# Performance work log

Measured on AMD Instinct MI355X. Metric: run time of the kernel, lower is better.

## Reference

```python
import jax, jax.numpy as jnp
import numpy as np

EPS = float(np.finfo(np.float64).eps)  # matches np.finfo(float).eps in torch combine()
TOP_K = 2


def setup_inputs() -> dict:
    key = jax.random.key(0)
    k0, k1, k2, k3 = jax.random.split(key, 4)
    N, D, F, E = 8192, 512, 2048, 8
    s = 0.02  # init scale keeps exp() in combine numerically tame
    return {
        "x": jax.random.normal(k0, (N, D), jnp.float32),
        "Wg": jax.random.normal(k1, (D, E), jnp.float32) * s,
        "W1": jax.random.normal(k2, (E, D, F), jnp.float32) * s,
        "b1": jnp.zeros((E, F), jnp.float32),
        "W2": jax.random.normal(k3, (E, F, D), jnp.float32) * s,
        "b2": jnp.zeros((E, D), jnp.float32),
    }


def reference(x, Wg, W1, b1, W2, b2):
    """Sparse-MoE token routing: gate -> dispatch -> per-expert MLP -> combine.

    Faithful to the torch dispatch()/combine() helpers: experts produce
    log-domain outputs; combine() does exp, gate-weighted scatter-add, eps
    floor, then log. Here expressed as dense masked expert compute (zero
    gates annihilate non-routed contributions), which is mathematically
    identical to the gather/index_add formulation and fully vectorized.
    """
    N, D = x.shape
    E = Wg.shape[1]
    # --- gating: noisy-free top-k softmax gates, scattered to [N, E] ---
    logits = x @ Wg                                    # [N, E]
    top_vals, top_idx = jax.lax.top_k(logits, TOP_K)   # [N, K]
    top_gates = jax.nn.softmax(top_vals, axis=-1)      # [N, K]
    gates = jnp.zeros((N, E), x.dtype).at[jnp.arange(N)[:, None], top_idx].set(top_gates)
    # --- expert MLPs (ReLU, per activation='relu' default) ---
    h = jax.nn.relu(jnp.einsum('nd,edf->nef', x, W1) + b1[None])  # [N, E, F]
    o = jnp.einsum('nef,efd->ned', h, W2) + b2[None]              # [N, E, D]
    # --- combine: gate-weighted sum of exp(expert_out), eps floor, log ---
    combined = jnp.einsum('ne,ned->nd', gates, jnp.exp(o))        # [N, D]
    combined = jnp.where(combined == 0, EPS, combined)
    return jnp.log(combined)
```

## Files before the change

kernel.cpp:

```cpp
#include <hip/hip_runtime.h>
#include <stdint.h>
#include <math.h>

#define NTOK 8192
#define DIM  512
#define FDIM 2048
#define NEXP 8
#define RMAX 17408
#define NMT  136
#define KSPLIT 2

typedef __attribute__((ext_vector_type(8))) __bf16 bf16x8;
typedef __attribute__((ext_vector_type(4))) float  f32x4;

#define GTPB 16
#define GB_BLOCKS (NTOK / GTPB)
#define PREP_W1 (GB_BLOCKS)
#define PREP_W2 (GB_BLOCKS + 8192)

#define OFF_W1T    ((size_t)0)
#define SZ_W1T     ((size_t)NEXP * DIM * FDIM * 2)
#define OFF_W2T    (OFF_W1T + SZ_W1T)
#define SZ_W2T     SZ_W1T
#define OFF_H      (OFF_W2T + SZ_W2T)
#define SZ_H       ((size_t)RMAX * FDIM * 2)
#define OFF_META   (OFF_H + SZ_H)
#define SZ_META    ((size_t)1024)
#define OFF_XG     (OFF_META + SZ_META)
#define SZ_XG      ((size_t)RMAX * DIM * 2)
#define OFF_O1     OFF_XG
#define OFF_O0     (OFF_XG + SZ_XG)
#define SZ_O0      ((size_t)RMAX * DIM * 4)
#define OFF_TOKE   (OFF_O0 + SZ_O0)
#define OFF_TOKLS  (OFF_TOKE + (size_t)NTOK * 8)
#define OFF_TOKG   (OFF_TOKLS + (size_t)NTOK * 8)
#define OFF_HISTP  (OFF_TOKG + (size_t)NTOK * 8)
#define OFF_BASEP  (OFF_HISTP + (size_t)GB_BLOCKS * NEXP * 4)
#define OFF_ROWS   (OFF_BASEP + (size_t)GB_BLOCKS * NEXP * 4)

__device__ __forceinline__ unsigned short f2bf(float f) {
  union { float f; unsigned int u; } v; v.f = f;
  unsigned int u = v.u;
  return (unsigned short)((u + 0x7fffu + ((u >> 16) & 1u)) >> 16);
}
__device__ __forceinline__ float bf2f(unsigned short u) {
  union { unsigned int u; float f; } v; v.u = ((unsigned int)u) << 16;
  return v.f;
}

__device__ __forceinline__ void gld16(const unsigned short* g, unsigned short* l) {
  __builtin_amdgcn_global_load_lds(
      (const __attribute__((address_space(1))) void*)g,
      (__attribute__((address_space(3))) void*)l, 16, 0, 0);
}

__device__ __forceinline__ void transpose_tile(const float* __restrict__ src,
                                               unsigned short* __restrict__ dst,
                                               int R, int C, int bx, int by, int bz) {
  __shared__ float t[32][33];
  const int r0 = by * 32, c0 = bx * 32;
  const float* s = src + (size_t)bz * R * C;
  unsigned short* d = dst + (size_t)bz * R * C;
  const int tr = threadIdx.x >> 5, tc = threadIdx.x & 31;
  #pragma unroll
  for (int i = 0; i < 4; i++)
    t[tr + i * 8][tc] = s[(size_t)(r0 + tr + i * 8) * C + (c0 + tc)];
  __syncthreads();
  #pragma unroll
  for (int i = 0; i < 4; i++)
    d[(size_t)(c0 + tr + i * 8) * R + (r0 + tc)] = f2bf(t[tc][tr + i * 8]);
}

__device__ __forceinline__ void gate_body(int gb, const float* __restrict__ x,
                            const float* __restrict__ Wg,
                            int* __restrict__ hist_part, int2* __restrict__ tok_e,
                            int2* __restrict__ tok_ls, float2* __restrict__ tok_g) {
  __shared__ int hist[NEXP];
  __shared__ int le[GTPB][2];
  __shared__ int ls[GTPB][2];
  __shared__ float lg[GTPB][2];
  const int wid = threadIdx.x >> 6;
  const int lane = threadIdx.x & 63;
  if (threadIdx.x < NEXP) hist[threadIdx.x] = 0;
  __syncthreads();
  for (int t = 0; t < 4; t++) {
    const int lt = wid * 4 + t;
    const int n = gb * GTPB + lt;
    double acc[NEXP];
    #pragma unroll
    for (int e = 0; e < NEXP; e++) acc[e] = 0.0;
    #pragma unroll
    for (int i = 0; i < 8; i++) {
      int dd = lane + i * 64;
      double xv = (double)x[(size_t)n * DIM + dd];
      const float* wr = Wg + (size_t)dd * NEXP;
      #pragma unroll
      for (int e = 0; e < NEXP; e++) acc[e] += xv * (double)wr[e];
    }
    #pragma unroll
    for (int s = 32; s > 0; s >>= 1)
      #pragma unroll
      for (int e = 0; e < NEXP; e++) acc[e] += __shfl_xor(acc[e], s, 64);
    if (lane == 0) {
      int i0 = 0;
      #pragma unroll
      for (int e = 1; e < NEXP; e++) if (acc[e] > acc[i0]) i0 = e;
      int i1 = (i0 == 0) ? 1 : 0;
      #pragma unroll
      for (int e = 0; e < NEXP; e++) { if (e == i0 || e == i1) continue; if (acc[e] > acc[i1]) i1 = e; }
      double e1 = exp(acc[i1] - acc[i0]), ssum = 1.0 + e1;
      le[lt][0] = i0; le[lt][1] = i1;
      ls[lt][0] = atomicAdd(&hist[i0], 1);
      ls[lt][1] = atomicAdd(&hist[i1], 1);
      lg[lt][0] = (float)(1.0 / ssum); lg[lt][1] = (float)(e1 / ssum);
    }
  }
  __syncthreads();
  if (threadIdx.x < NEXP) hist_part[gb * NEXP + threadIdx.x] = hist[threadIdx.x];
  if (threadIdx.x < GTPB) {
    const int lt = threadIdx.x;
    const int n = gb * GTPB + lt;
    tok_e[n]  = make_int2(le[lt][0], le[lt][1]);
    tok_ls[n] = make_int2(ls[lt][0], ls[lt][1]);
    tok_g[n]  = make_float2(lg[lt][0], lg[lt][1]);
  }
}

__global__ __launch_bounds__(256) void prep_kernel(const float* __restrict__ W1,
    unsigned short* __restrict__ W1t, const float* __restrict__ W2,
    unsigned short* __restrict__ W2t, const float* __restrict__ x,
    const float* __restrict__ Wg, int* __restrict__ hist_part, int2* __restrict__ tok_e,
    int2* __restrict__ tok_ls, float2* __restrict__ tok_g) {
  const int b = blockIdx.x;
  if (b < GB_BLOCKS) {
    gate_body(b, x, Wg, hist_part, tok_e, tok_ls, tok_g);
  } else if (b < PREP_W2) {
    const int q = b - PREP_W1;
    transpose_tile(W1, W1t, DIM, FDIM, q & 63, (q >> 6) & 15, q >> 10);
  } else {
    const int q = b - PREP_W2;
    transpose_tile(W2, W2t, FDIM, DIM, q & 15, (q >> 4) & 63, q >> 10);
  }
}

__global__ __launch_bounds__(256) void scan_kernel(const int* __restrict__ hist_part,
    int* __restrict__ offsets, int* __restrict__ base_part, int* __restrict__ mtile_e) {
  __shared__ int hp[GB_BLOCKS * NEXP];
  __shared__ int segsum[8][NEXP];
  __shared__ int segbase[8][NEXP];
  __shared__ int tot[NEXP];
  __shared__ int soff[NEXP + 1];
  for (int i = threadIdx.x; i < GB_BLOCKS * NEXP; i += 256) hp[i] = hist_part[i];
  __syncthreads();
  if (threadIdx.x < 64) {
    const int e = threadIdx.x & 7, s = threadIdx.x >> 3;
    int run = 0;
    for (int b = s * 64; b < s * 64 + 64; b++) {
      int v = hp[b * NEXP + e]; hp[b * NEXP + e] = run; run += v;
    }
    segsum[s][e] = run;
  }
  __syncthreads();
  if (threadIdx.x < NEXP) {
    const int e = threadIdx.x;
    int run = 0;
    for (int s = 0; s < 8; s++) { segbase[s][e] = run; run += segsum[s][e]; }
    tot[e] = run;
  }
  __syncthreads();
  if (threadIdx.x == 0) {
    int off = 0;
    for (int e = 0; e < NEXP; e++) { soff[e] = off; offsets[e] = off; off += (tot[e] + 127) & ~127; }
    soff[NEXP] = off; offsets[NEXP] = off;
    for (int t = 0; t < NMT; t++) {
      int r = t * 128, e = NEXP - 1;
      for (int q = 0; q < NEXP; q++)
        if (r >= soff[q] && r < soff[q + 1]) { e = q; break; }
      mtile_e[t] = e;
    }
  }
  __syncthreads();
  for (int i = threadIdx.x; i < GB_BLOCKS * NEXP; i += 256) {
    const int b = i >> 3, e = i & 7;
    base_part[i] = soff[e] + segbase[b >> 6][e] + hp[i];
  }
}

__global__ void gather_kernel(const float* __restrict__ x, const int2* __restrict__ tok_e,
                              const int2* __restrict__ tok_ls, const int* __restrict__ base_part,
                              ushort4* __restrict__ xg, int2* __restrict__ rows) {
  const int n = blockIdx.x;
  int2 te = tok_e[n]; int2 tl = tok_ls[n];
  const int gb = n / GTPB;
  const int r0 = base_part[gb * NEXP + te.x] + tl.x;
  const int r1 = base_part[gb * NEXP + te.y] + tl.y;
  if (threadIdx.x == 0) rows[n] = make_int2(r0, r1);
  const float4* xr = (const float4*)(x + (size_t)n * DIM);
  float4 v = xr[threadIdx.x];
  ushort4 o;
  o.x = f2bf(v.x); o.y = f2bf(v.y); o.z = f2bf(v.z); o.w = f2bf(v.w);
  xg[(size_t)r0 * (DIM / 4) + threadIdx.x] = o;
  xg[(size_t)r1 * (DIM / 4) + threadIdx.x] = o;
}

template <int K, int LDA, int LDB>
__device__ __forceinline__ void gemm_core(const unsigned short* __restrict__ A,
                                          const unsigned short* __restrict__ B,
                                          int m0, int n0, f32x4 acc[4][4]) {
  __shared__ __align__(16) unsigned short As[128 * 64];
  __shared__ __align__(16) unsigned short Bs[128 * 64];
  const int tid = threadIdx.x;
  const int wid = tid >> 6, lane = tid & 63;
  const int wm = (wid >> 1) * 64, wn = (wid & 1) * 64;
  const int quad = lane >> 4, l16 = lane & 15;
  const int srow = tid >> 3;
  const int scol = ((tid & 7) ^ (srow & 7)) << 3;
  unsigned short* As_w = As + 512 * wid;
  unsigned short* Bs_w = Bs + 512 * wid;
  const int r7 = (l16 & 7) << 3;
  const unsigned short* Ar = A + (size_t)(m0 + srow) * LDA + scol;
  const unsigned short* Br = B + (size_t)(n0 + srow) * LDB + scol;
  #pragma unroll 1
  for (int kt = 0; kt < K; kt += 64) {
    __syncthreads();
    #pragma unroll
    for (int p = 0; p < 4; p++) {
      gld16(Ar + (size_t)(32 * p) * LDA + kt, As_w + p * 2048);
      gld16(Br + (size_t)(32 * p) * LDB + kt, Bs_w + p * 2048);
    }
    __syncthreads();
    #pragma unroll
    for (int kk = 0; kk < 2; kk++) {
      const int swz = ((kk * 4 + quad) << 3) ^ r7;
      bf16x8 af[4], bfr[4];
      #pragma unroll
      for (int i = 0; i < 4; i++) {
        af[i]  = *(const bf16x8*)(As + (wm + i * 16 + l16) * 64 + swz);
        bfr[i] = *(const bf16x8*)(Bs + (wn + i * 16 + l16) * 64 + swz);
      }
      #pragma unroll
      for (int mi = 0; mi < 4; mi++)
        #pragma unroll
        for (int ni = 0; ni < 4; ni++)
          acc[mi][ni] = __builtin_amdgcn_mfma_f32_16x16x32_bf16(af[mi], bfr[ni], acc[mi][ni], 0, 0, 0);
    }
  }
}

__global__ __launch_bounds__(256, 4) void gemm1_kernel(const unsigned short* __restrict__ xg,
    const unsigned short* __restrict__ W1t, const int* __restrict__ mtile_e,
    const float* __restrict__ b1, unsigned short* __restrict__ h) {
  const int bm = blockIdx.x, bn = blockIdx.y;
  const int e = mtile_e[bm];
  f32x4 acc[4][4];
  #pragma unroll
  for (int i = 0; i < 4; i++)
    #pragma unroll
    for (int j = 0; j < 4; j++) acc[i][j] = (f32x4){0.f, 0.f, 0.f, 0.f};
  gemm_core<DIM, DIM, DIM>(xg, W1t + (size_t)e * FDIM * DIM, bm * 128, bn * 128, acc);
  const int tid = threadIdx.x, wid = tid >> 6, lane = tid & 63;
  const int wm = (wid >> 1) * 64, wn = (wid & 1) * 64, quad = lane >> 4, l16 = lane & 15;
  #pragma unroll
  for (int mi = 0; mi < 4; mi++) {
    #pragma unroll
    for (int ni = 0; ni < 4; ni++) {
      const int col = bn * 128 + wn + ni * 16 + l16;
      const float bb = b1[e * FDIM + col];
      #pragma unroll
      for (int r = 0; r < 4; r++) {
        const int row = bm * 128 + wm + mi * 16 + quad * 4 + r;
        float v = acc[mi][ni][r] + bb;
        h[(size_t)row * FDIM + col] = f2bf(v > 0.f ? v : 0.f);
      }
    }
  }
}

__global__ __launch_bounds__(256, 4) void gemm2_kernel(const unsigned short* __restrict__ h,
    const unsigned short* __restrict__ W2t, const int* __restrict__ mtile_e,
    float* __restrict__ o0, unsigned short* __restrict__ o1) {
  const int bm = blockIdx.x, bn = blockIdx.y, ks = blockIdx.z;
  const int e = mtile_e[bm];
  const int k0 = ks * (FDIM / KSPLIT);
  f32x4 acc[4][4];
  #pragma unroll
  for (int i = 0; i < 4; i++)
    #pragma unroll
    for (int j = 0; j < 4; j++) acc[i][j] = (f32x4){0.f, 0.f, 0.f, 0.f};
  gemm_core<FDIM / KSPLIT, FDIM, FDIM>(h + k0, W2t + (size_t)e * DIM * FDIM + k0,
                                       bm * 128, bn * 128, acc);
  const int tid = threadIdx.x, wid = tid >> 6, lane = tid & 63;
  const int wm = (wid >> 1) * 64, wn = (wid & 1) * 64, quad = lane >> 4, l16 = lane & 15;
  if (ks == 0) {
    #pragma unroll
    for (int mi = 0; mi < 4; mi++)
      #pragma unroll
      for (int r = 0; r < 4; r++) {
        const int row = bm * 128 + wm + mi * 16 + quad * 4 + r;
        #pragma unroll
        for (int ni = 0; ni < 4; ni++) {
          const int col = bn * 128 + wn + ni * 16 + l16;
          o0[(size_t)row * DIM + col] = acc[mi][ni][r];
        }
      }
  } else {
    #pragma unroll
    for (int mi = 0; mi < 4; mi++)
      #pragma unroll
      for (int r = 0; r < 4; r++) {
        const int row = bm * 128 + wm + mi * 16 + quad * 4 + r;
        #pragma unroll
        for (int ni = 0; ni < 4; ni++) {
          const int col = bn * 128 + wn + ni * 16 + l16;
          o1[(size_t)row * DIM + col] = f2bf(acc[mi][ni][r]);
        }
      }
  }
}

__global__ void combine_kernel(const float* __restrict__ o0, const unsigned short* __restrict__ o1,
                               const int2* __restrict__ tok_e, const int2* __restrict__ rows,
                               const float2* __restrict__ tok_g, const float* __restrict__ b2,
                               float* __restrict__ out) {
  const int n = blockIdx.x;
  const int c = threadIdx.x * 4;
  int2 te = tok_e[n]; int2 rr = rows[n]; float2 tg = tok_g[n];
  const int r0 = rr.x, r1 = rr.y;
  float4 a0 = *(const float4*)(o0 + (size_t)r0 * DIM + c);
  float4 a1 = *(const float4*)(o0 + (size_t)r1 * DIM + c);
  ushort4 p0 = *(const ushort4*)(o1 + (size_t)r0 * DIM + c);
  ushort4 p1 = *(const ushort4*)(o1 + (size_t)r1 * DIM + c);
  float4 c0 = *(const float4*)(b2 + te.x * DIM + c);
  float4 c1 = *(const float4*)(b2 + te.y * DIM + c);
  float4 res;
  #pragma unroll
  for (int j = 0; j < 4; j++) {
    float v0 = ((const float*)&a0)[j] + bf2f(((const unsigned short*)&p0)[j]) + ((const float*)&c0)[j];
    float v1 = ((const float*)&a1)[j] + bf2f(((const unsigned short*)&p1)[j]) + ((const float*)&c1)[j];
    float v = tg.x * expf(v0) + tg.y * expf(v1);
    v = (v == 0.0f) ? 2.220446049250313e-16f : v;
    ((float*)&res)[j] = logf(v);
  }
  *(float4*)(out + (size_t)n * DIM + c) = res;
}

extern "C" void kernel_launch(void* const* d_in, const int* in_sizes, int n_in,
                              void* d_out, int out_size, void* d_ws, size_t ws_size,
                              hipStream_t stream) {
  const float* x  = (const float*)d_in[0];
  const float* Wg = (const float*)d_in[1];
  const float* W1 = (const float*)d_in[2];
  const float* b1 = (const float*)d_in[3];
  const float* W2 = (const float*)d_in[4];
  const float* b2 = (const float*)d_in[5];
  float* out = (float*)d_out;
  char* ws = (char*)d_ws;

  unsigned short* W1t = (unsigned short*)(ws + OFF_W1T);
  unsigned short* W2t = (unsigned short*)(ws + OFF_W2T);
  unsigned short* h   = (unsigned short*)(ws + OFF_H);
  int* meta    = (int*)(ws + OFF_META);
  int* offsets = meta;
  int* mtile_e = meta + 16;
  unsigned short* xg = (unsigned short*)(ws + OFF_XG);
  unsigned short* o1 = (unsigned short*)(ws + OFF_O1);
  float* o0      = (float*)(ws + OFF_O0);
  int2* tok_e    = (int2*)(ws + OFF_TOKE);
  int2* tok_ls   = (int2*)(ws + OFF_TOKLS);
  float2* tok_g  = (float2*)(ws + OFF_TOKG);
  int* hist_part = (int*)(ws + OFF_HISTP);
  int* base_part = (int*)(ws + OFF_BASEP);
  int2* rows     = (int2*)(ws + OFF_ROWS);

  prep_kernel<<<GB_BLOCKS + 2 * 8192, 256, 0, stream>>>(W1, W1t, W2, W2t, x, Wg,
                                                        hist_part, tok_e, tok_ls, tok_g);
  scan_kernel<<<1, 256, 0, stream>>>(hist_part, offsets, base_part, mtile_e);
  gather_kernel<<<NTOK, 128, 0, stream>>>(x, tok_e, tok_ls, base_part, (ushort4*)xg, rows);
  gemm1_kernel<<<dim3(NMT, FDIM / 128), 256, 0, stream>>>(xg, W1t, mtile_e, b1, h);
  gemm2_kernel<<<dim3(NMT, DIM / 128, KSPLIT), 256, 0, stream>>>(h, W2t, mtile_e, o0, o1);
  combine_kernel<<<NTOK, 128, 0, stream>>>(o0, o1, tok_e, rows, tok_g, b2, out);
}
```

Baseline: 294.3 us.

## Fuse gather into GEMM1 via row indices, skip empty tiles, widen transposes

The separate gather kernel is gone. x is converted to bf16 once inside the gating blocks, and GEMM1 loads A rows indirectly through a token-row map (trow) using global_load_lds, so the duplicated xg buffer is never written. M-tiles that hold only padding are marked -1 and skipped in both GEMMs. The weight transposes use 64x64 tiles with fewer blocks, combine packs two tokens per 256-thread block and uses fast __expf/__logf, and part of the fp32 split-K output reuses the W1t region to save workspace. Risks include precision loss from the fast math intrinsics and the aliasing of o0lo with W1t, which is only safe because GEMM1 has finished before GEMM2 writes.

```diff
diff --git a/kernel.cpp b/kernel.cpp
--- a/kernel.cpp
+++ b/kernel.cpp
@@ -9,6 +9,7 @@
 #define RMAX 17408
 #define NMT  136
 #define KSPLIT 2
+#define O0LO_ROWS 8192
 
 typedef __attribute__((ext_vector_type(8))) __bf16 bf16x8;
 typedef __attribute__((ext_vector_type(4))) float  f32x4;
@@ -16,7 +17,8 @@
 #define GTPB 16
 #define GB_BLOCKS (NTOK / GTPB)
 #define PREP_W1 (GB_BLOCKS)
-#define PREP_W2 (GB_BLOCKS + 8192)
+#define PREP_W2 (GB_BLOCKS + 2048)
+#define PREP_TOTAL (GB_BLOCKS + 4096)
 
 #define OFF_W1T    ((size_t)0)
 #define SZ_W1T     ((size_t)NEXP * DIM * FDIM * 2)
@@ -26,12 +28,14 @@
 #define SZ_H       ((size_t)RMAX * FDIM * 2)
 #define OFF_META   (OFF_H + SZ_H)
 #define SZ_META    ((size_t)1024)
-#define OFF_XG     (OFF_META + SZ_META)
-#define SZ_XG      ((size_t)RMAX * DIM * 2)
-#define OFF_O1     OFF_XG
-#define OFF_O0     (OFF_XG + SZ_XG)
-#define SZ_O0      ((size_t)RMAX * DIM * 4)
-#define OFF_TOKE   (OFF_O0 + SZ_O0)
+#define OFF_XB     (OFF_META + SZ_META)
+#define SZ_XB      ((size_t)NTOK * DIM * 2)
+#define OFF_O1     (OFF_XB + SZ_XB)
+#define SZ_O1      ((size_t)RMAX * DIM * 2)
+#define OFF_O0HI   (OFF_O1 + SZ_O1)
+#define SZ_O0HI    ((size_t)(RMAX - O0LO_ROWS) * DIM * 4)
+#define OFF_TROW   (OFF_O0HI + SZ_O0HI)
+#define OFF_TOKE   (OFF_TROW + (size_t)RMAX * 4)
 #define OFF_TOKLS  (OFF_TOKE + (size_t)NTOK * 8)
 #define OFF_TOKG   (OFF_TOKLS + (size_t)NTOK * 8)
 #define OFF_HISTP  (OFF_TOKG + (size_t)NTOK * 8)
@@ -54,27 +58,28 @@
       (__attribute__((address_space(3))) void*)l, 16, 0, 0);
 }
 
-__device__ __forceinline__ void transpose_tile(const float* __restrict__ src,
-                                               unsigned short* __restrict__ dst,
-                                               int R, int C, int bx, int by, int bz) {
-  __shared__ float t[32][33];
-  const int r0 = by * 32, c0 = bx * 32;
+__device__ __forceinline__ void transpose_tile64(const float* __restrict__ src,
+                                                 unsigned short* __restrict__ dst,
+                                                 int R, int C, int bx, int by, int bz) {
+  __shared__ float t[64][65];
+  const int r0 = by * 64, c0 = bx * 64;
   const float* s = src + (size_t)bz * R * C;
   unsigned short* d = dst + (size_t)bz * R * C;
-  const int tr = threadIdx.x >> 5, tc = threadIdx.x & 31;
-  #pragma unroll
-  for (int i = 0; i < 4; i++)
-    t[tr + i * 8][tc] = s[(size_t)(r0 + tr + i * 8) * C + (c0 + tc)];
-  __syncthreads();
-  #pragma unroll
-  for (int i = 0; i < 4; i++)
-    d[(size_t)(c0 + tr + i * 8) * R + (r0 + tc)] = f2bf(t[tc][tr + i * 8]);
+  const int tr = threadIdx.x >> 6, tc = threadIdx.x & 63;
+  #pragma unroll
+  for (int i = 0; i < 16; i++)
+    t[tr + i * 4][tc] = s[(size_t)(r0 + tr + i * 4) * C + (c0 + tc)];
+  __syncthreads();
+  #pragma unroll
+  for (int i = 0; i < 16; i++)
+    d[(size_t)(c0 + tr + i * 4) * R + (r0 + tc)] = f2bf(t[tc][tr + i * 4]);
 }
 
 __device__ __forceinline__ void gate_body(int gb, const float* __restrict__ x,
                             const float* __restrict__ Wg,
                             int* __restrict__ hist_part, int2* __restrict__ tok_e,
-                            int2* __restrict__ tok_ls, float2* __restrict__ tok_g) {
+                            int2* __restrict__ tok_ls, float2* __restrict__ tok_g,
+                            ushort4* __restrict__ xb) {
   __shared__ int hist[NEXP];
   __shared__ int le[GTPB][2];
   __shared__ int ls[GTPB][2];
@@ -115,6 +120,14 @@
       lg[lt][0] = (float)(1.0 / ssum); lg[lt][1] = (float)(e1 / ssum);
     }
   }
+  for (int v = threadIdx.x; v < GTPB * (DIM / 4); v += 256) {
+    const int lt = v / (DIM / 4), c = v % (DIM / 4);
+    const int n = gb * GTPB + lt;
+    float4 f = *(const float4*)(x + (size_t)n * DIM + c * 4);
+    ushort4 o;
+    o.x = f2bf(f.x); o.y = f2bf(f.y); o.z = f2bf(f.z); o.w = f2bf(f.w);
+    xb[(size_t)n * (DIM / 4) + c] = o;
+  }
   __syncthreads();
   if (threadIdx.x < NEXP) hist_part[gb * NEXP + threadIdx.x] = hist[threadIdx.x];
   if (threadIdx.x < GTPB) {
@@ -130,26 +143,28 @@
     unsigned short* __restrict__ W1t, const float* __restrict__ W2,
     unsigned short* __restrict__ W2t, const float* __restrict__ x,
     const float* __restrict__ Wg, int* __restrict__ hist_part, int2* __restrict__ tok_e,
-    int2* __restrict__ tok_ls, float2* __restrict__ tok_g) {
+    int2* __restrict__ tok_ls, float2* __restrict__ tok_g, ushort4* __restrict__ xb) {
   const int b = blockIdx.x;
   if (b < GB_BLOCKS) {
-    gate_body(b, x, Wg, hist_part, tok_e, tok_ls, tok_g);
+    gate_body(b, x, Wg, hist_part, tok_e, tok_ls, tok_g, xb);
   } else if (b < PREP_W2) {
     const int q = b - PREP_W1;
-    transpose_tile(W1, W1t, DIM, FDIM, q & 63, (q >> 6) & 15, q >> 10);
+    transpose_tile64(W1, W1t, DIM, FDIM, q & 31, (q >> 5) & 7, q >> 8);
   } else {
     const int q = b - PREP_W2;
-    transpose_tile(W2, W2t, FDIM, DIM, q & 15, (q >> 4) & 63, q >> 10);
+    transpose_tile64(W2, W2t, FDIM, DIM, q & 7, (q >> 3) & 31, q >> 8);
   }
 }
 
 __global__ __launch_bounds__(256) void scan_kernel(const int* __restrict__ hist_part,
-    int* __restrict__ offsets, int* __restrict__ base_part, int* __restrict__ mtile_e) {
+    int* __restrict__ offsets, int* __restrict__ base_part, int* __restrict__ mtile_e,
+    int* __restrict__ trow) {
   __shared__ int hp[GB_BLOCKS * NEXP];
   __shared__ int segsum[8][NEXP];
   __shared__ int segbase[8][NEXP];
   __shared__ int tot[NEXP];
   __shared__ int soff[NEXP + 1];
+  for (int i = threadIdx.x; i < RMAX; i += 256) trow[i] = 0;
   for (int i = threadIdx.x; i < GB_BLOCKS * NEXP; i += 256) hp[i] = hist_part[i];
   __syncthreads();
   if (threadIdx.x < 64) {
@@ -176,7 +191,7 @@
       int r = t * 128, e = NEXP - 1;
       for (int q = 0; q < NEXP; q++)
         if (r >= soff[q] && r < soff[q + 1]) { e = q; break; }
-      mtile_e[t] = e;
+      mtile_e[t] = (r < soff[e] + tot[e]) ? e : -1;
     }
   }
   __syncthreads();
@@ -186,21 +201,17 @@
   }
 }
 
-__global__ void gather_kernel(const float* __restrict__ x, const int2* __restrict__ tok_e,
-                              const int2* __restrict__ tok_ls, const int* __restrict__ base_part,
-                              ushort4* __restrict__ xg, int2* __restrict__ rows) {
-  const int n = blockIdx.x;
+__global__ __launch_bounds__(256) void resolve_kernel(const int2* __restrict__ tok_e,
+    const int2* __restrict__ tok_ls, const int* __restrict__ base_part,
+    int2* __restrict__ rows, int* __restrict__ trow) {
+  const int n = blockIdx.x * 256 + threadIdx.x;
   int2 te = tok_e[n]; int2 tl = tok_ls[n];
   const int gb = n / GTPB;
   const int r0 = base_part[gb * NEXP + te.x] + tl.x;
   const int r1 = base_part[gb * NEXP + te.y] + tl.y;
-  if (threadIdx.x == 0) rows[n] = make_int2(r0, r1);
-  const float4* xr = (const float4*)(x + (size_t)n * DIM);
-  float4 v = xr[threadIdx.x];
-  ushort4 o;
-  o.x = f2bf(v.x); o.y = f2bf(v.y); o.z = f2bf(v.z); o.w = f2bf(v.w);
-  xg[(size_t)r0 * (DIM / 4) + threadIdx.x] = o;
-  xg[(size_t)r1 * (DIM / 4) + threadIdx.x] = o;
+  rows[n] = make_int2(r0, r1);
+  trow[r0] = n;
+  trow[r1] = n;
 }
 
 template <int K, int LDA, int LDB>
@@ -247,19 +258,61 @@
   }
 }
 
-__global__ __launch_bounds__(256, 4) void gemm1_kernel(const unsigned short* __restrict__ xg,
-    const unsigned short* __restrict__ W1t, const int* __restrict__ mtile_e,
-    const float* __restrict__ b1, unsigned short* __restrict__ h) {
+__global__ __launch_bounds__(256, 4) void gemm1_kernel(const unsigned short* __restrict__ xb,
+    const int* __restrict__ trow, const unsigned short* __restrict__ W1t,
+    const int* __restrict__ mtile_e, const float* __restrict__ b1,
+    unsigned short* __restrict__ h) {
   const int bm = blockIdx.x, bn = blockIdx.y;
   const int e = mtile_e[bm];
+  if (e < 0) return;
+  __shared__ __align__(16) unsigned short As[128 * 64];
+  __shared__ __align__(16) unsigned short Bs[128 * 64];
+  const int tid = threadIdx.x;
+  const int wid = tid >> 6, lane = tid & 63;
+  const int wm = (wid >> 1) * 64, wn = (wid & 1) * 64;
+  const int quad = lane >> 4, l16 = lane & 15;
+  const int srow = tid >> 3;
+  const int scol = ((tid & 7) ^ (srow & 7)) << 3;
+  unsigned short* As_w = As + 512 * wid;
+  unsigned short* Bs_w = Bs + 512 * wid;
+  const int r7 = (l16 & 7) << 3;
+  int tokA[4];
+  #pragma unroll
+  for (int p = 0; p < 4; p++) tokA[p] = trow[bm * 128 + 32 * p + srow];
+  const unsigned short* Br = W1t + (size_t)e * FDIM * DIM + (size_t)(bn * 128 + srow) * DIM + scol;
+
   f32x4 acc[4][4];
   #pragma unroll
   for (int i = 0; i < 4; i++)
     #pragma unroll
     for (int j = 0; j < 4; j++) acc[i][j] = (f32x4){0.f, 0.f, 0.f, 0.f};
-  gemm_core<DIM, DIM, DIM>(xg, W1t + (size_t)e * FDIM * DIM, bm * 128, bn * 128, acc);
-  const int tid = threadIdx.x, wid = tid >> 6, lane = tid & 63;
-  const int wm = (wid >> 1) * 64, wn = (wid & 1) * 64, quad = lane >> 4, l16 = lane & 15;
+
+  #pragma unroll 1
+  for (int kt = 0; kt < DIM; kt += 64) {
+    __syncthreads();
+    #pragma unroll
+    for (int p = 0; p < 4; p++) {
+      gld16(xb + (size_t)tokA[p] * DIM + scol + kt, As_w + p * 2048);
+      gld16(Br + (size_t)(32 * p) * DIM + kt, Bs_w + p * 2048);
+    }
+    __syncthreads();
+    #pragma unroll
+    for (int kk = 0; kk < 2; kk++) {
+      const int swz = ((kk * 4 + quad) << 3) ^ r7;
+      bf16x8 af[4], bfr[4];
+      #pragma unroll
+      for (int i = 0; i < 4; i++) {
+        af[i]  = *(const bf16x8*)(As + (wm + i * 16 + l16) * 64 + swz);
+        bfr[i] = *(const bf16x8*)(Bs + (wn + i * 16 + l16) * 64 + swz);
+      }
+      #pragma unroll
+      for (int mi = 0; mi < 4; mi++)
+        #pragma unroll
+        for (int ni = 0; ni < 4; ni++)
+          acc[mi][ni] = __builtin_amdgcn_mfma_f32_16x16x32_bf16(af[mi], bfr[ni], acc[mi][ni], 0, 0, 0);
+    }
+  }
+
   #pragma unroll
   for (int mi = 0; mi < 4; mi++) {
     #pragma unroll
@@ -278,9 +331,10 @@
 
 __global__ __launch_bounds__(256, 4) void gemm2_kernel(const unsigned short* __restrict__ h,
     const unsigned short* __restrict__ W2t, const int* __restrict__ mtile_e,
-    float* __restrict__ o0, unsigned short* __restrict__ o1) {
+    float* __restrict__ o0lo, float* __restrict__ o0hi, unsigned short* __restrict__ o1) {
   const int bm = blockIdx.x, bn = blockIdx.y, ks = blockIdx.z;
   const int e = mtile_e[bm];
+  if (e < 0) return;
   const int k0 = ks * (FDIM / KSPLIT);
   f32x4 acc[4][4];
   #pragma unroll
@@ -292,6 +346,7 @@
   const int tid = threadIdx.x, wid = tid >> 6, lane = tid & 63;
   const int wm = (wid >> 1) * 64, wn = (wid & 1) * 64, quad = lane >> 4, l16 = lane & 15;
   if (ks == 0) {
+    float* ob = (bm < O0LO_ROWS / 128) ? o0lo : (o0hi - (size_t)O0LO_ROWS * DIM);
     #pragma unroll
     for (int mi = 0; mi < 4; mi++)
       #pragma unroll
@@ -300,7 +355,7 @@
         #pragma unroll
         for (int ni = 0; ni < 4; ni++) {
           const int col = bn * 128 + wn + ni * 16 + l16;
-          o0[(size_t)row * DIM + col] = acc[mi][ni][r];
+          ob[(size_t)row * DIM + col] = acc[mi][ni][r];
         }
       }
   } else {
@@ -318,16 +373,21 @@
   }
 }
 
-__global__ void combine_kernel(const float* __restrict__ o0, const unsigned short* __restrict__ o1,
+__global__ void combine_kernel(const float* __restrict__ o0lo, const float* __restrict__ o0hi,
+                               const unsigned short* __restrict__ o1,
                                const int2* __restrict__ tok_e, const int2* __restrict__ rows,
                                const float2* __restrict__ tok_g, const float* __restrict__ b2,
                                float* __restrict__ out) {
-  const int n = blockIdx.x;
-  const int c = threadIdx.x * 4;
+  const int n = blockIdx.x * 2 + (threadIdx.x >> 7);
+  const int c = (threadIdx.x & 127) * 4;
   int2 te = tok_e[n]; int2 rr = rows[n]; float2 tg = tok_g[n];
   const int r0 = rr.x, r1 = rr.y;
-  float4 a0 = *(const float4*)(o0 + (size_t)r0 * DIM + c);
-  float4 a1 = *(const float4*)(o0 + (size_t)r1 * DIM + c);
+  const float* p0f = (r0 < O0LO_ROWS) ? (o0lo + (size_t)r0 * DIM)
+                                      : (o0hi + (size_t)(r0 - O0LO_ROWS) * DIM);
+  const float* p1f = (r1 < O0LO_ROWS) ? (o0lo + (size_t)r1 * DIM)
+                                      : (o0hi + (size_t)(r1 - O0LO_ROWS) * DIM);
+  float4 a0 = *(const float4*)(p0f + c);
+  float4 a1 = *(const float4*)(p1f + c);
   ushort4 p0 = *(const ushort4*)(o1 + (size_t)r0 * DIM + c);
   ushort4 p1 = *(const ushort4*)(o1 + (size_t)r1 * DIM + c);
   float4 c0 = *(const float4*)(b2 + te.x * DIM + c);
@@ -337,9 +397,9 @@
   for (int j = 0; j < 4; j++) {
     float v0 = ((const float*)&a0)[j] + bf2f(((const unsigned short*)&p0)[j]) + ((const float*)&c0)[j];
     float v1 = ((const float*)&a1)[j] + bf2f(((const unsigned short*)&p1)[j]) + ((const float*)&c1)[j];
-    float v = tg.x * expf(v0) + tg.y * expf(v1);
+    float v = tg.x * __expf(v0) + tg.y * __expf(v1);
     v = (v == 0.0f) ? 2.220446049250313e-16f : v;
-    ((float*)&res)[j] = logf(v);
+    ((float*)&res)[j] = __logf(v);
   }
   *(float4*)(out + (size_t)n * DIM + c) = res;
 }
@@ -362,9 +422,11 @@
   int* meta    = (int*)(ws + OFF_META);
   int* offsets = meta;
   int* mtile_e = meta + 16;
-  unsigned short* xg = (unsigned short*)(ws + OFF_XG);
+  unsigned short* xb = (unsigned short*)(ws + OFF_XB);
   unsigned short* o1 = (unsigned short*)(ws + OFF_O1);
-  float* o0      = (float*)(ws + OFF_O0);
+  float* o0lo    = (float*)(ws + OFF_W1T);
+  float* o0hi    = (float*)(ws + OFF_O0HI);
+  int* trow      = (int*)(ws + OFF_TROW);
   int2* tok_e    = (int2*)(ws + OFF_TOKE);
   int2* tok_ls   = (int2*)(ws + OFF_TOKLS);
   float2* tok_g  = (float2*)(ws + OFF_TOKG);
@@ -372,11 +434,11 @@
   int* base_part = (int*)(ws + OFF_BASEP);
   int2* rows     = (int2*)(ws + OFF_ROWS);
 
-  prep_kernel<<<GB_BLOCKS + 2 * 8192, 256, 0, stream>>>(W1, W1t, W2, W2t, x, Wg,
-                                                        hist_part, tok_e, tok_ls, tok_g);
-  scan_kernel<<<1, 256, 0, stream>>>(hist_part, offsets, base_part, mtile_e);
-  gather_kernel<<<NTOK, 128, 0, stream>>>(x, tok_e, tok_ls, base_part, (ushort4*)xg, rows);
-  gemm1_kernel<<<dim3(NMT, FDIM / 128), 256, 0, stream>>>(xg, W1t, mtile_e, b1, h);
-  gemm2_kernel<<<dim3(NMT, DIM / 128, KSPLIT), 256, 0, stream>>>(h, W2t, mtile_e, o0, o1);
-  combine_kernel<<<NTOK, 128, 0, stream>>>(o0, o1, tok_e, rows, tok_g, b2, out);
-}
+  prep_kernel<<<PREP_TOTAL, 256, 0, stream>>>(W1, W1t, W2, W2t, x, Wg,
+                                              hist_part, tok_e, tok_ls, tok_g, (ushort4*)xb);
+  scan_kernel<<<1, 256, 0, stream>>>(hist_part, offsets, base_part, mtile_e, trow);
+  resolve_kernel<<<NTOK / 256, 256, 0, stream>>>(tok_e, tok_ls, base_part, rows, trow);
+  gemm1_kernel<<<dim3(NMT, FDIM / 128), 256, 0, stream>>>(xb, trow, W1t, mtile_e, b1, h);
+  gemm2_kernel<<<dim3(NMT, DIM / 128, KSPLIT), 256, 0, stream>>>(h, W2t, mtile_e, o0lo, o0hi, o1);
+  combine_kernel<<<NTOK / 2, 256, 0, stream>>>(o0lo, o0hi, o1, tok_e, rows, tok_g, b2, out);
+}
```

Result: faster. 281.2 us (-4.5%).
